# Kernel tuning notes

Hardware: AMD Instinct MI355X
Metric: run time of the kernel (lower is better)

The kernel has to match this reference:

```python
import jax, jax.numpy as jnp
import numpy as np

B, K, V = 32, 2048, 60000
D, H, L, NB = 512, 8, 4, 5
DH, M = D // H, 256  # dim_head, num random features
EPS_K = 1e-4


def _ln(x, g, b, eps=1e-5):
    mu = x.mean(-1, keepdims=True)
    var = ((x - mu) ** 2).mean(-1, keepdims=True)
    return (x - mu) / jnp.sqrt(var + eps) * g + b


def _favor_feats(x, proj, is_query):
    # FAVOR+ positive softmax-kernel features (lucidrains performer)
    dn = x.shape[-1] ** -0.25
    xd = x * dn
    dd = jnp.einsum('bhnd,md->bhnm', xd, proj)
    diag = 0.5 * jnp.sum(xd * xd, -1, keepdims=True)
    mx = jnp.max(dd, -1, keepdims=True) if is_query else jnp.max(dd)
    return (proj.shape[0] ** -0.5) * (jnp.exp(dd - diag - mx) + EPS_K)


def _orth_proj(m, d, rng):
    # gaussian orthogonal random matrix (scaling=0: chi row norms)
    blocks = []
    for _ in range(-(-m // d)):
        q, _ = np.linalg.qr(rng.standard_normal((d, d)))
        blocks.append(q.T)
    mat = np.concatenate(blocks)[:m]
    mult = np.linalg.norm(rng.standard_normal((m, d)), axis=1)
    return (mult[:, None] * mat).astype(np.float32)


def setup_inputs() -> dict:
    rng = np.random.default_rng(0)
    w = lambda *s: jnp.asarray(rng.standard_normal(s).astype(np.float32) * 0.02)
    return dict(
        expr=jnp.asarray(rng.random((B, K)).astype(np.float32)),
        coords=jnp.asarray(rng.standard_normal((B, 2)).astype(np.float32)),
        gene_ids=jnp.arange(K, dtype=jnp.int32),
        gene_table=w(V, D), pos_table=w(K, D), value_table=w(NB, D),
        sp_w=w(2, D), sp_b=jnp.zeros(D), sp_ln_g=jnp.ones(D), sp_ln_b=jnp.zeros(D),
        ln1_g=jnp.ones((L, D)), ln1_b=jnp.zeros((L, D)),
        qw=w(L, D, D), qb=jnp.zeros((L, D)), kw=w(L, D, D), kb=jnp.zeros((L, D)),
        vw=w(L, D, D), vb=jnp.zeros((L, D)), ow=w(L, D, D), ob=jnp.zeros((L, D)),
        proj=jnp.asarray(np.stack([_orth_proj(M, DH, rng) for _ in range(L)])),
        ln2_g=jnp.ones((L, D)), ln2_b=jnp.zeros((L, D)),
        ff1_w=w(L, D, 4 * D), ff1_b=jnp.zeros((L, 4 * D)),
        ff2_w=w(L, 4 * D, D), ff2_b=jnp.zeros((L, D)),
        cq_w=w(D, D), cq_b=jnp.zeros(D), ck_w=w(D, D), ck_b=jnp.zeros(D),
        cv_w=w(D, D), cv_b=jnp.zeros(D), co_w=w(D, D), co_b=jnp.zeros(D),
    )


def reference(expr, coords, gene_ids, gene_table, pos_table, value_table,
              sp_w, sp_b, sp_ln_g, sp_ln_b, ln1_g, ln1_b, qw, qb, kw, kb,
              vw, vb, ow, ob, proj, ln2_g, ln2_b, ff1_w, ff1_b, ff2_w, ff2_b,
              cq_w, cq_b, ck_w, ck_b, cv_w, cv_b, co_w, co_b):
    b, k = expr.shape
    bins = jnp.clip((expr * NB).astype(jnp.int32), 0, NB - 1)
    gene_embeds = gene_table[gene_ids][None] + pos_table[None, :k] + value_table[bins]
    sp = jax.nn.gelu(_ln(coords @ sp_w + sp_b, sp_ln_g, sp_ln_b), approximate=False)
    x = jnp.concatenate([sp[:, None, :], gene_embeds], axis=1)  # (B, K+1, D)
    n = k + 1
    for l in range(L):
        h = _ln(x, ln1_g[l], ln1_b[l])
        q = (h @ qw[l] + qb[l]).reshape(b, n, H, DH).transpose(0, 2, 1, 3)
        kk = (h @ kw[l] + kb[l]).reshape(b, n, H, DH).transpose(0, 2, 1, 3)
        v = (h @ vw[l] + vb[l]).reshape(b, n, H, DH).transpose(0, 2, 1, 3)
        qp = _favor_feats(q, proj[l], True)   # (b,h,n,M)
        kp = _favor_feats(kk, proj[l], False)
        dinv = 1.0 / jnp.einsum('bhnm,bhm->bhn', qp, kp.sum(axis=2))
        ctx = jnp.einsum('bhnm,bhnd->bhmd', kp, v)
        o = jnp.einsum('bhnm,bhmd->bhnd', qp, ctx) * dinv[..., None]
        o = o.transpose(0, 2, 1, 3).reshape(b, n, D)
        x = x + (o @ ow[l] + ob[l])
        h = _ln(x, ln2_g[l], ln2_b[l])
        x = x + jax.nn.gelu(h @ ff1_w[l] + ff1_b[l], approximate=False) @ ff2_w[l] + ff2_b[l]
    qc = x[:, :1] @ cq_w + cq_b
    kc = x[:, 1:] @ ck_w + ck_b
    vc = x[:, 1:] @ cv_w + cv_b
    attn = jax.nn.softmax(jnp.einsum('bqd,bkd->bqk', qc, kc) / (D ** 0.5), axis=-1)
    pooled = jnp.einsum('bqk,bkd->bqd', attn, vc)[:, 0]
    return pooled @ co_w + co_b
```

## Files before the change

### kernel.cpp

```cpp
#include <hip/hip_runtime.h>
#include <hip/hip_bf16.h>

#define BB 32
#define KK 2048
#define NTOK 2049
#define DD 512
#define NH 8
#define DHD 64
#define NL 4
#define MM 256
#define RTOT (BB*NTOK)
#define HROWS (RTOT/2)
#define DN 0.35355339059327373f
#define RM 0.0625f
#define EPSK 1e-4f

typedef __attribute__((ext_vector_type(8))) short bf16x8;
typedef __attribute__((ext_vector_type(4))) float f32x4;

__device__ __forceinline__ float wsum(float v) {
#pragma unroll
  for (int o = 32; o; o >>= 1) v += __shfl_xor(v, o);
  return v;
}
__device__ __forceinline__ float wmax(float v) {
#pragma unroll
  for (int o = 32; o; o >>= 1) v = fmaxf(v, __shfl_xor(v, o));
  return v;
}
__device__ __forceinline__ float gelu1(float v) {
  return 0.5f * v * (1.0f + erff(v * 0.70710678118654752f));
}
__device__ __forceinline__ float b2f(unsigned short u) {
  union { unsigned int i; float f; } w; w.i = ((unsigned int)u) << 16; return w.f;
}
__device__ __forceinline__ unsigned short f2b(float f) {
  union { float f; unsigned int i; } w; w.f = f;
  unsigned int r = w.i + 0x7FFFu + ((w.i >> 16) & 1u);
  return (unsigned short)(r >> 16);
}
__device__ __forceinline__ float4 ld4(const float* p) { return *(const float4*)p; }
__device__ __forceinline__ float4 ld4(const unsigned short* p) {
  ushort4 u = *(const ushort4*)p;
  return make_float4(b2f(u.x), b2f(u.y), b2f(u.z), b2f(u.w));
}
__device__ __forceinline__ void st4(float* p, float4 v) { *(float4*)p = v; }
__device__ __forceinline__ void st4(unsigned short* p, float4 v) {
  ushort4 u; u.x = f2b(v.x); u.y = f2b(v.y); u.z = f2b(v.z); u.w = f2b(v.w);
  *(ushort4*)p = u;
}
__device__ __forceinline__ bf16x8 ld8s(const unsigned short* p) {
  union { ushort4 u[2]; bf16x8 v; } w;
  w.u[0] = *(const ushort4*)p;
  w.u[1] = *(const ushort4*)(p + 4);
  return w.v;
}
__device__ __forceinline__ void gload16(const void* g, void* l) {
  __builtin_amdgcn_global_load_lds(
      (const __attribute__((address_space(1))) void*)g,
      (__attribute__((address_space(3))) void*)l, 16, 0, 0);
}

__global__ void sentinel_k(float* out, int n) {
  int i = blockIdx.x * 256 + threadIdx.x;
  if (i < n) out[i] = 12345.0f;
}

__global__ void biaspack_k(const float* __restrict__ a, const float* __restrict__ bsrc,
                           float* __restrict__ dst) {
  int i = threadIdx.x;
  dst[i] = a[i]; dst[i + 256] = a[i + 256];
  dst[512 + i] = bsrc[i]; dst[768 + i] = bsrc[i + 256];
}

__global__ __launch_bounds__(256) void wcvt_k(const float* __restrict__ W,
    unsigned short* __restrict__ Wt, int Kd, int Cols) {
  __shared__ float Ls[64][65];
  int tid = threadIdx.x;
  int n0 = blockIdx.x * 64, k0 = blockIdx.y * 64;
  int kr = tid >> 2, nseg = (tid & 3) << 4;
#pragma unroll
  for (int u = 0; u < 4; ++u) {
    float4 v = *(const float4*)(W + (size_t)(k0 + kr) * Cols + n0 + nseg + u * 4);
    *(float4*)&Ls[kr][nseg + u * 4] = v;
  }
  __syncthreads();
  int nr = tid >> 2, kseg = (tid & 3) << 4;
  unsigned int pk[8];
#pragma unroll
  for (int i = 0; i < 8; ++i) {
    unsigned short lo = f2b(Ls[kseg + 2 * i][nr]);
    unsigned short hi = f2b(Ls[kseg + 2 * i + 1][nr]);
    pk[i] = (unsigned int)lo | ((unsigned int)hi << 16);
  }
  unsigned short* dst = Wt + (size_t)(n0 + nr) * Kd + k0 + kseg;
  ((uint4*)dst)[0] = make_uint4(pk[0], pk[1], pk[2], pk[3]);
  ((uint4*)dst)[1] = make_uint4(pk[4], pk[5], pk[6], pk[7]);
}

__global__ __launch_bounds__(256) void embed_k(const float* __restrict__ expr,
    const int* __restrict__ gene_ids, const float* __restrict__ gene_table,
    const float* __restrict__ pos_table, const float* __restrict__ value_tab,
    float* __restrict__ x) {
  int tok = blockIdx.x * 2 + (threadIdx.x >> 7);
  int t = threadIdx.x & 127;
  int b = tok >> 11;
  int k = tok & 2047;
  float e = expr[tok];
  int bin = (int)(e * 5.0f);
  bin = bin < 0 ? 0 : (bin > 4 ? 4 : bin);
  int g = gene_ids[k];
  float4 a = ((const float4*)(gene_table + (size_t)g * DD))[t];
  float4 p = ((const float4*)(pos_table + (size_t)k * DD))[t];
  float4 vv = ((const float4*)(value_tab + (size_t)bin * DD))[t];
  float4 r;
  r.x = a.x + p.x + vv.x; r.y = a.y + p.y + vv.y;
  r.z = a.z + p.z + vv.z; r.w = a.w + p.w + vv.w;
  ((float4*)(x + ((size_t)b * NTOK + 1 + k) * DD))[t] = r;
}

__global__ __launch_bounds__(256) void sp_k(const float* __restrict__ coords,
    const float* __restrict__ sp_w, const float* __restrict__ sp_b,
    const float* __restrict__ g, const float* __restrict__ bb,
    float* __restrict__ x) {
  int b = blockIdx.x, t = threadIdx.x;
  __shared__ float red[8];
  float c0 = coords[2 * b], c1 = coords[2 * b + 1];
  float v0 = fmaf(c0, sp_w[t],       fmaf(c1, sp_w[512 + t], sp_b[t]));
  float v1 = fmaf(c0, sp_w[t + 256], fmaf(c1, sp_w[768 + t], sp_b[t + 256]));
  float s = wsum(v0 + v1);
  int wid = t >> 6;
  if ((t & 63) == 0) red[wid] = s;
  __syncthreads();
  float mu = (red[0] + red[1] + red[2] + red[3]) * (1.0f / 512.0f);
  float d0 = v0 - mu, d1 = v1 - mu;
  float s2 = wsum(d0 * d0 + d1 * d1);
  if ((t & 63) == 0) red[4 + wid] = s2;
  __syncthreads();
  float var = (red[4] + red[5] + red[6] + red[7]) * (1.0f / 512.0f);
  float rs = rsqrtf(var + 1e-5f);
  float y0 = d0 * rs * g[t] + bb[t];
  float y1 = d1 * rs * g[t + 256] + bb[t + 256];
  x[(size_t)b * NTOK * DD + t] = gelu1(y0);
  x[(size_t)b * NTOK * DD + t + 256] = gelu1(y1);
}

__global__ __launch_bounds__(128) void ln_k(const float* __restrict__ x,
    const float* __restrict__ gamma, const float* __restrict__ beta,
    unsigned short* __restrict__ h) {
  size_t row = blockIdx.x;
  int t = threadIdx.x;
  float4 v = ((const float4*)(x + row * DD))[t];
  float s = v.x + v.y + v.z + v.w;
  float s2 = v.x * v.x + v.y * v.y + v.z * v.z + v.w * v.w;
  __shared__ float red[4];
  float ws1 = wsum(s), ws2 = wsum(s2);
  int wid = t >> 6;
  if ((t & 63) == 0) { red[wid * 2] = ws1; red[wid * 2 + 1] = ws2; }
  __syncthreads();
  float S = red[0] + red[2], S2 = red[1] + red[3];
  float mu = S * (1.0f / 512.0f);
  float var = S2 * (1.0f / 512.0f) - mu * mu;
  float rs = rsqrtf(var + 1e-5f);
  float4 gm = ((const float4*)gamma)[t], bt = ((const float4*)beta)[t];
  float4 o;
  o.x = (v.x - mu) * rs * gm.x + bt.x;
  o.y = (v.y - mu) * rs * gm.y + bt.y;
  o.z = (v.z - mu) * rs * gm.z + bt.z;
  o.w = (v.w - mu) * rs * gm.w + bt.w;
  st4(h + row * DD + t * 4, o);
}

__global__ __launch_bounds__(256) void cvt_k(const float* __restrict__ x,
    unsigned short* __restrict__ o, size_t n8) {
  size_t i = (size_t)blockIdx.x * 256 + threadIdx.x;
  if (i >= n8) return;
  float4 a = ((const float4*)x)[2 * i];
  float4 b = ((const float4*)x)[2 * i + 1];
  st4(o + i * 8, a);
  st4(o + i * 8 + 4, b);
}

template <typename TC, int FLAGS>
__global__ __launch_bounds__(256) void gemm_bb(const unsigned short* __restrict__ A, long lda,
    const unsigned short* __restrict__ Wt, const float* __restrict__ bias,
    TC* __restrict__ C, int ldc, int R, int Kd) {
  __shared__ unsigned short Sh[128 * 136];
  unsigned short* As = Sh;
  unsigned short* Bs = Sh + 128 * 64;
  const int tid = threadIdx.x;
  const int lane = tid & 63;
  const int w = tid >> 6;
  const int wr = w >> 1, wc = w & 1;
  const int nwg = gridDim.x * gridDim.y;
  const int orig = blockIdx.y * gridDim.x + blockIdx.x;
  const int qd = nwg >> 3, rm = nwg & 7;
  const int xcd = orig & 7, idx = orig >> 3;
  const int wg = (xcd < rm ? xcd * (qd + 1) : rm * (qd + 1) + (xcd - rm) * qd) + idx;
  const int rblk = (wg / gridDim.x) << 7;
  const int cblk = (wg % gridDim.x) << 7;
  const int m0 = lane & 15, kb = lane >> 4;
  const int lrow8 = lane >> 3;
  const int csw = (((lane & 7) ^ lrow8) << 3);
  f32x4 acc[4][4] = {};
  for (int k0 = 0; k0 < Kd; k0 += 64) {
#pragma unroll
    for (int rd = 0; rd < 4; ++rd) {
      int rg = w * 32 + rd * 8;
      int gra = rblk + rg + lrow8; if (gra >= R) gra = R - 1;
      gload16(A  + (size_t)gra * lda + k0 + csw, &As[rg * 64]);
      gload16(Wt + (size_t)(cblk + rg + lrow8) * Kd + k0 + csw, &Bs[rg * 64]);
    }
    __syncthreads();
    bf16x8 af[2][4], bfr[2][4];
#pragma unroll
    for (int ks = 0; ks < 2; ++ks) {
      int c = (ks << 2) | kb;
#pragma unroll
      for (int mi = 0; mi < 4; ++mi) {
        int ar = wr * 64 + mi * 16 + m0;
        af[ks][mi] = *(const bf16x8*)&As[ar * 64 + ((c ^ (ar & 7)) << 3)];
        int br = wc * 64 + mi * 16 + m0;
        bfr[ks][mi] = *(const bf16x8*)&Bs[br * 64 + ((c ^ (br & 7)) << 3)];
      }
    }
#pragma unroll
    for (int ks = 0; ks < 2; ++ks)
#pragma unroll
      for (int mi = 0; mi < 4; ++mi)
#pragma unroll
        for (int ni = 0; ni < 4; ++ni)
          acc[mi][ni] = __builtin_amdgcn_mfma_f32_16x16x32_bf16(af[ks][mi], bfr[ks][ni], acc[mi][ni], 0, 0, 0);
    __syncthreads();
  }
  const int lrow4 = (lane >> 4) << 2, lcol = lane & 15;
  if constexpr (sizeof(TC) == 2) {
#pragma unroll
    for (int mi = 0; mi < 4; ++mi)
#pragma unroll
      for (int reg = 0; reg < 4; ++reg) {
        int rloc = wr * 64 + mi * 16 + lrow4 + reg;
#pragma unroll
        for (int ni = 0; ni < 4; ++ni) {
          int cloc = wc * 64 + ni * 16 + lcol;
          float v = acc[mi][ni][reg] + bias[cblk + cloc];
          if constexpr ((FLAGS & 1) != 0) v = gelu1(v);
          Sh[rloc * 136 + cloc] = f2b(v);
        }
      }
    __syncthreads();
    int rl = tid >> 1;
    int row = rblk + rl;
    if (row < R) {
      unsigned short* cp = (unsigned short*)C + (size_t)row * ldc + cblk;
#pragma unroll
      for (int u = 0; u < 8; ++u) {
        int c = (tid & 1) * 8 + u * 16;
        *(uint4*)(cp + c) = *(const uint4*)&Sh[rl * 136 + c];
      }
    }
  } else {
    float* Sf = (float*)Sh;
#pragma unroll
    for (int p = 0; p < 2; ++p) {
      if (wr == p) {
#pragma unroll
        for (int mi = 0; mi < 4; ++mi)
#pragma unroll
          for (int reg = 0; reg < 4; ++reg) {
            int rloc = mi * 16 + lrow4 + reg;
#pragma unroll
            for (int ni = 0; ni < 4; ++ni) {
              int cloc = wc * 64 + ni * 16 + lcol;
              float v = acc[mi][ni][reg] + bias[cblk + cloc];
              if constexpr ((FLAGS & 1) != 0) v = gelu1(v);
              Sf[rloc * 132 + cloc] = v;
            }
          }
      }
      __syncthreads();
      int rl = tid >> 2;
      int row = rblk + p * 64 + rl;
      if (row < R) {
        float* cp = (float*)C + (size_t)row * ldc + cblk;
#pragma unroll
        for (int u = 0; u < 8; ++u) {
          int c = (tid & 3) * 4 + u * 16;
          float4 nv = *(const float4*)&Sf[rl * 132 + c];
          if constexpr ((FLAGS & 2) != 0) {
            float4 old = *(const float4*)(cp + c);
            nv.x += old.x; nv.y += old.y; nv.z += old.z; nv.w += old.w;
          }
          *(float4*)(cp + c) = nv;
        }
      }
      __syncthreads();
    }
  }
}

template <typename TA, typename TC>
__global__ __launch_bounds__(256) void gemm_t(const TA* __restrict__ A, long lda,
    const float* __restrict__ W, const float* __restrict__ bias,
    TC* __restrict__ C, int ldc, int R, int Kd, int Cols) {
  __shared__ float As[16][68];
  __shared__ float Ws[16][64];
  int tid = threadIdx.x;
  int tx = tid & 15, ty = tid >> 4;
  int rblk = blockIdx.y << 6, cblk = blockIdx.x << 6;
  float acc[4][4] = {};
  int lr = tid >> 2, lk = (tid & 3) << 2;
  int wk = tid >> 4, wcc = (tid & 15) << 2;
  int gra = rblk + lr;
  for (int k0 = 0; k0 < Kd; k0 += 16) {
    float4 av = make_float4(0.f, 0.f, 0.f, 0.f);
    if (gra < R) av = ld4(A + (size_t)gra * lda + k0 + lk);
    As[lk][lr] = av.x; As[lk + 1][lr] = av.y; As[lk + 2][lr] = av.z; As[lk + 3][lr] = av.w;
    *(float4*)&Ws[wk][wcc] = *(const float4*)(W + (size_t)(k0 + wk) * Cols + cblk + wcc);
    __syncthreads();
#pragma unroll
    for (int p = 0; p < 16; ++p) {
      float4 a4 = *(const float4*)&As[p][ty << 2];
      float4 b4 = *(const float4*)&Ws[p][tx << 2];
      acc[0][0] = fmaf(a4.x, b4.x, acc[0][0]); acc[0][1] = fmaf(a4.x, b4.y, acc[0][1]);
      acc[0][2] = fmaf(a4.x, b4.z, acc[0][2]); acc[0][3] = fmaf(a4.x, b4.w, acc[0][3]);
      acc[1][0] = fmaf(a4.y, b4.x, acc[1][0]); acc[1][1] = fmaf(a4.y, b4.y, acc[1][1]);
      acc[1][2] = fmaf(a4.y, b4.z, acc[1][2]); acc[1][3] = fmaf(a4.y, b4.w, acc[1][3]);
      acc[2][0] = fmaf(a4.z, b4.x, acc[2][0]); acc[2][1] = fmaf(a4.z, b4.y, acc[2][1]);
      acc[2][2] = fmaf(a4.z, b4.z, acc[2][2]); acc[2][3] = fmaf(a4.z, b4.w, acc[2][3]);
      acc[3][0] = fmaf(a4.w, b4.x, acc[3][0]); acc[3][1] = fmaf(a4.w, b4.y, acc[3][1]);
      acc[3][2] = fmaf(a4.w, b4.z, acc[3][2]); acc[3][3] = fmaf(a4.w, b4.w, acc[3][3]);
    }
    __syncthreads();
  }
  int gcb = cblk + (tx << 2);
  float4 bi = *(const float4*)(bias + gcb);
#pragma unroll
  for (int i = 0; i < 4; ++i) {
    int gr = rblk + (ty << 2) + i;
    if (gr < R) {
      float4 val;
      val.x = acc[i][0] + bi.x; val.y = acc[i][1] + bi.y;
      val.z = acc[i][2] + bi.z; val.w = acc[i][3] + bi.w;
      TC* cp = C + (size_t)gr * ldc + gcb;
      st4(cp, val);
    }
  }
}

__global__ __launch_bounds__(256) void kmax_k(const unsigned short* __restrict__ kv,
    const unsigned short* __restrict__ projb, float* __restrict__ bmax) {
  int orig = blockIdx.y * gridDim.x + blockIdx.x;
  int wg = ((orig & 7) << 7) + (orig >> 3);
  int bh = wg >> 2, gy = wg & 3;
  int b = bh >> 3, hh = bh & 7;
  int tid = threadIdx.x;
  int lane = tid & 63, w = tid >> 6;
  int m0 = lane & 15, kb = lane >> 4;
  __shared__ float red[4];
  bf16x8 bp[4][2];
#pragma unroll
  for (int nf = 0; nf < 4; ++nf)
#pragma unroll
    for (int ks = 0; ks < 2; ++ks)
      bp[nf][ks] = *(const bf16x8*)(projb + (size_t)(w * 64 + nf * 16 + m0) * 64 + ks * 32 + kb * 8);
  const unsigned short* kvb = kv + (size_t)b * NTOK * 1024 + hh * 64;
  float mx = -1e30f;
  for (int t = gy; t < 65; t += 4) {
    int n0 = t * 32;
    bf16x8 aq[2][2];
#pragma unroll
    for (int mi = 0; mi < 2; ++mi) {
      int n = n0 + mi * 16 + m0; if (n >= NTOK) n = NTOK - 1;
#pragma unroll
      for (int ks = 0; ks < 2; ++ks)
        aq[mi][ks] = *(const bf16x8*)(kvb + (size_t)n * 1024 + ks * 32 + kb * 8);
    }
    f32x4 da[2][4] = {};
#pragma unroll
    for (int ks = 0; ks < 2; ++ks)
#pragma unroll
      for (int mi = 0; mi < 2; ++mi)
#pragma unroll
        for (int nf = 0; nf < 4; ++nf)
          da[mi][nf] = __builtin_amdgcn_mfma_f32_16x16x32_bf16(aq[mi][ks], bp[nf][ks], da[mi][nf], 0, 0, 0);
#pragma unroll
    for (int mi = 0; mi < 2; ++mi)
#pragma unroll
      for (int nf = 0; nf < 4; ++nf)
#pragma unroll
        for (int r = 0; r < 4; ++r)
          mx = fmaxf(mx, da[mi][nf][r]);
  }
  mx *= DN;
  mx = wmax(mx);
  if ((tid & 63) == 0) red[tid >> 6] = mx;
  __syncthreads();
  if (tid == 0)
    bmax[(size_t)bh * 4 + gy] = fmaxf(fmaxf(red[0], red[1]), fmaxf(red[2], red[3]));
}

__global__ __launch_bounds__(256) void maxred_k(const float* __restrict__ in, int n,
                                                float* __restrict__ out) {
  float m = -1e30f;
  for (int i = threadIdx.x; i < n; i += 256) m = fmaxf(m, in[i]);
  m = wmax(m);
  __shared__ float red[4];
  if ((threadIdx.x & 63) == 0) red[threadIdx.x >> 6] = m;
  __syncthreads();
  if (threadIdx.x == 0) out[0] = fmaxf(fmaxf(red[0], red[1]), fmaxf(red[2], red[3]));
}

__global__ __launch_bounds__(256) void k2_k(const unsigned short* __restrict__ kv,
    const unsigned short* __restrict__ projb,
    const float* __restrict__ kmaxg, unsigned short* __restrict__ ctxTb,
    float* __restrict__ kpsum) {
  int orig = blockIdx.y * gridDim.x + blockIdx.x;
  int wg = ((orig & 7) << 7) + (orig >> 3);
  int bh = wg >> 2, mg = wg & 3;
  int b = bh >> 3, hh = bh & 7;
  int tid = threadIdx.x;
  int lane = tid & 63, w = tid >> 6;
  int m0 = lane & 15, kb = lane >> 4;
  __shared__ __align__(16) unsigned short kpT[64 * 44];
  __shared__ __align__(16) unsigned short VT[64 * 44];
  float kmax = kmaxg[0];
  bf16x8 bp[2];
#pragma unroll
  for (int ks = 0; ks < 2; ++ks)
    bp[ks] = *(const bf16x8*)(projb + (size_t)(mg * 64 + w * 16 + m0) * 64 + ks * 32 + kb * 8);
  f32x4 acc[4] = {};
  float ksum = 0.f;
  int dv = tid & 63, tq = tid >> 6;
  const unsigned short* kvb = kv + (size_t)b * NTOK * 1024 + hh * 64;
  for (int t = 0; t < 65; ++t) {
    int n0 = t * 32;
    int tlim = NTOK - n0; if (tlim > 32) tlim = 32;
    __syncthreads();
    {
      unsigned int pk[4];
#pragma unroll
      for (int j = 0; j < 8; ++j) {
        int n = n0 + tq * 8 + j; if (n >= NTOK) n = NTOK - 1;
        unsigned int v = kvb[(size_t)n * 1024 + 512 + dv];
        if (j & 1) pk[j >> 1] |= v << 16; else pk[j >> 1] = v;
      }
      *(uint2*)&VT[dv * 44 + tq * 8]     = make_uint2(pk[0], pk[1]);
      *(uint2*)&VT[dv * 44 + tq * 8 + 4] = make_uint2(pk[2], pk[3]);
    }
    bf16x8 aq[2][2];
    float dg[2];
#pragma unroll
    for (int mi = 0; mi < 2; ++mi) {
      int n = n0 + mi * 16 + m0; if (n >= NTOK) n = NTOK - 1;
      float s = 0.f;
#pragma unroll
      for (int ks = 0; ks < 2; ++ks) {
        aq[mi][ks] = *(const bf16x8*)(kvb + (size_t)n * 1024 + ks * 32 + kb * 8);
        const unsigned short* ap = (const unsigned short*)&aq[mi][ks];
#pragma unroll
        for (int j = 0; j < 8; ++j) { float v = b2f(ap[j]); s = fmaf(v, v, s); }
      }
      s += __shfl_xor(s, 16);
      s += __shfl_xor(s, 32);
      dg[mi] = 0.5f * DN * DN * s;
    }
    f32x4 da[2] = {};
#pragma unroll
    for (int ks = 0; ks < 2; ++ks)
#pragma unroll
      for (int mi = 0; mi < 2; ++mi)
        da[mi] = __builtin_amdgcn_mfma_f32_16x16x32_bf16(aq[mi][ks], bp[ks], da[mi], 0, 0, 0);
#pragma unroll
    for (int mi = 0; mi < 2; ++mi) {
      unsigned int pk[2];
#pragma unroll
      for (int r = 0; r < 4; ++r) {
        float dval = __shfl(dg[mi], (kb << 2) | r);
        int tt = mi * 16 + (kb << 2) + r;
        float kp = 0.f;
        if (tt < tlim)
          kp = RM * (__expf(da[mi][r] * DN - dval - kmax) + EPSK);
        ksum += kp;
        unsigned int h = (unsigned int)f2b(kp);
        if (r & 1) pk[r >> 1] |= h << 16; else pk[r >> 1] = h;
      }
      *(uint2*)&kpT[(w * 16 + m0) * 44 + mi * 16 + (kb << 2)] = make_uint2(pk[0], pk[1]);
    }
    __syncthreads();
    bf16x8 af = ld8s(&kpT[(w * 16 + m0) * 44 + kb * 8]);
#pragma unroll
    for (int di = 0; di < 4; ++di) {
      bf16x8 bfv = ld8s(&VT[(di * 16 + m0) * 44 + kb * 8]);
      acc[di] = __builtin_amdgcn_mfma_f32_16x16x32_bf16(af, bfv, acc[di], 0, 0, 0);
    }
  }
  ksum += __shfl_xor(ksum, 16);
  ksum += __shfl_xor(ksum, 32);
  if (kb == 0) kpsum[(size_t)bh * MM + mg * 64 + w * 16 + m0] = ksum;
  unsigned short* cT = ctxTb + (size_t)bh * (64 * 256);
#pragma unroll
  for (int di = 0; di < 4; ++di)
#pragma unroll
    for (int r = 0; r < 4; ++r) {
      int m = mg * 64 + w * 16 + (kb << 2) + r;
      int d = di * 16 + m0;
      cT[d * 256 + m] = f2b(acc[di][r]);
    }
}

__global__ __launch_bounds__(256) void qfeat_k(unsigned short* __restrict__ kv,
    const unsigned short* __restrict__ projb,
    const unsigned short* __restrict__ ctxTb,
    const float* __restrict__ kpsum) {
  int orig = blockIdx.y * gridDim.x + blockIdx.x;
  int wg = ((orig & 7) * 416) + (orig >> 3);
  int bh = wg / 13, gy = wg % 13;
  int b = bh >> 3, hh = bh & 7;
  int tid = threadIdx.x;
  int lane = tid & 63, w = tid >> 6;
  int m0 = lane & 15, kb = lane >> 4;
  __shared__ float ddl[32 * 266];
  __shared__ unsigned short Pb[32 * 264];
  __shared__ float ksum_s[256];
  __shared__ float diag_s[32];
  __shared__ float dinv_s[32];
  ksum_s[tid] = kpsum[(size_t)bh * MM + tid];
  bf16x8 bp[4][2], bc[8];
#pragma unroll
  for (int nf = 0; nf < 4; ++nf)
#pragma unroll
    for (int ks = 0; ks < 2; ++ks)
      bp[nf][ks] = *(const bf16x8*)(projb + (size_t)(w * 64 + nf * 16 + m0) * 64 + ks * 32 + kb * 8);
  const unsigned short* cT = ctxTb + (size_t)bh * (64 * 256);
#pragma unroll
  for (int ks = 0; ks < 8; ++ks)
    bc[ks] = *(const bf16x8*)(cT + (size_t)(w * 16 + m0) * 256 + ks * 32 + kb * 8);
  unsigned short* kvb = kv + (size_t)b * NTOK * 1024 + hh * 64;
  int t8 = tid >> 3, q8 = tid & 7;
  for (int t = gy; t < 65; t += 13) {
    int n0 = t * 32;
    int tlim = NTOK - n0; if (tlim > 32) tlim = 32;
    bf16x8 aq[2][2];
#pragma unroll
    for (int mi = 0; mi < 2; ++mi) {
      int n = n0 + mi * 16 + m0; if (n >= NTOK) n = NTOK - 1;
#pragma unroll
      for (int ks = 0; ks < 2; ++ks)
        aq[mi][ks] = *(const bf16x8*)(kvb + (size_t)n * 1024 + ks * 32 + kb * 8);
    }
#pragma unroll
    for (int mi = 0; mi < 2; ++mi) {
      float s = 0.f;
      const unsigned short* ap = (const unsigned short*)&aq[mi][0];
#pragma unroll
      for (int j = 0; j < 16; ++j) { float v = b2f(ap[j]); s = fmaf(v, v, s); }
      s += __shfl_xor(s, 16); s += __shfl_xor(s, 32);
      if (w == 0 && kb == 0) diag_s[mi * 16 + m0] = 0.5f * DN * DN * s;
    }
    f32x4 da[2][4] = {};
#pragma unroll
    for (int ks = 0; ks < 2; ++ks)
#pragma unroll
      for (int mi = 0; mi < 2; ++mi)
#pragma unroll
        for (int nf = 0; nf < 4; ++nf)
          da[mi][nf] = __builtin_amdgcn_mfma_f32_16x16x32_bf16(aq[mi][ks], bp[nf][ks], da[mi][nf], 0, 0, 0);
#pragma unroll
    for (int mi = 0; mi < 2; ++mi)
#pragma unroll
      for (int nf = 0; nf < 4; ++nf)
#pragma unroll
        for (int r = 0; r < 4; ++r)
          ddl[(mi * 16 + kb * 4 + r) * 266 + w * 64 + nf * 16 + m0] = da[mi][nf][r] * DN;
    __syncthreads();
    float mx = -1e30f;
    if (t8 < tlim) {
      for (int j = 0; j < 32; ++j) mx = fmaxf(mx, ddl[t8 * 266 + q8 + 8 * j]);
    }
    mx = fmaxf(mx, __shfl_xor(mx, 1));
    mx = fmaxf(mx, __shfl_xor(mx, 2));
    mx = fmaxf(mx, __shfl_xor(mx, 4));
    float den = 0.f;
    if (t8 < tlim) {
      float dg = diag_s[t8];
      for (int j = 0; j < 32; ++j) {
        int mm = q8 + 8 * j;
        float e = RM * (__expf(ddl[t8 * 266 + mm] - dg - mx) + EPSK);
        Pb[t8 * 264 + mm] = f2b(e);
        den = fmaf(e, ksum_s[mm], den);
      }
    }
    den += __shfl_xor(den, 1); den += __shfl_xor(den, 2); den += __shfl_xor(den, 4);
    if (q8 == 0 && t8 < tlim) dinv_s[t8] = 1.0f / den;
    __syncthreads();
    f32x4 oa[2] = {};
#pragma unroll
    for (int ks = 0; ks < 8; ++ks)
#pragma unroll
      for (int mi = 0; mi < 2; ++mi) {
        bf16x8 ap = *(const bf16x8*)&Pb[(mi * 16 + m0) * 264 + ks * 32 + kb * 8];
        oa[mi] = __builtin_amdgcn_mfma_f32_16x16x32_bf16(ap, bc[ks], oa[mi], 0, 0, 0);
      }
#pragma unroll
    for (int mi = 0; mi < 2; ++mi)
#pragma unroll
      for (int r = 0; r < 4; ++r) {
        int row = mi * 16 + kb * 4 + r;
        if (row < tlim) {
          kvb[(size_t)(n0 + row) * 1024 + 512 + w * 16 + m0] =
              f2b(oa[mi][r] * dinv_s[row]);
        }
      }
    __syncthreads();
  }
}

__global__ __launch_bounds__(256) void attn_sc_k(const unsigned short* __restrict__ qc,
    const unsigned short* __restrict__ kcvc, float* __restrict__ scbuf,
    float* __restrict__ pmax) {
  int b = blockIdx.x, g = blockIdx.y, tid = threadIdx.x;
  int w = tid >> 6, lane = tid & 63;
  __shared__ float qs[DD];
  __shared__ float red[4];
  {
    ushort2 qu = ((const ushort2*)(qc + (size_t)b * DD))[tid];
    ((float2*)qs)[tid] = make_float2(b2f(qu.x), b2f(qu.y));
  }
  __syncthreads();
  float mx = -1e30f;
  for (int it = 0; it < 64; ++it) {
    int kk = g * 256 + w * 64 + it;
    const unsigned short* row = kcvc + ((size_t)b * NTOK + 1 + kk) * 1024 + lane * 8;
    float4 r0 = ld4(row), r1 = ld4(row + 4);
    float4 q0 = ((const float4*)qs)[lane * 2], q1 = ((const float4*)qs)[lane * 2 + 1];
    float s = r0.x * q0.x + r0.y * q0.y + r0.z * q0.z + r0.w * q0.w
            + r1.x * q1.x + r1.y * q1.y + r1.z * q1.z + r1.w * q1.w;
    s = wsum(s) * 0.044194173824159216f;
    if (lane == 0) scbuf[(size_t)b * KK + kk] = s;
    mx = fmaxf(mx, s);
  }
  if (lane == 0) red[w] = mx;
  __syncthreads();
  if (tid == 0) pmax[b * 8 + g] = fmaxf(fmaxf(red[0], red[1]), fmaxf(red[2], red[3]));
}
__global__ __launch_bounds__(256) void attn_w_k(const float* __restrict__ pmax,
    float* __restrict__ scbuf, float* __restrict__ pinv) {
  int b = blockIdx.x, tid = threadIdx.x;
  __shared__ float red[4];
  float mx = -1e30f;
#pragma unroll
  for (int i = 0; i < 8; ++i) mx = fmaxf(mx, pmax[b * 8 + i]);
  float sum = 0.f;
  for (int i = tid; i < KK; i += 256) {
    float e = __expf(scbuf[(size_t)b * KK + i] - mx);
    scbuf[(size_t)b * KK + i] = e;
    sum += e;
  }
  sum = wsum(sum);
  if ((tid & 63) == 0) red[tid >> 6] = sum;
  __syncthreads();
  if (tid == 0) pinv[b] = 1.0f / (red[0] + red[1] + red[2] + red[3]);
}
__global__ __launch_bounds__(256) void attn_vs_k(const float* __restrict__ scbuf,
    const unsigned short* __restrict__ kcvc, float* __restrict__ ppart) {
  int b = blockIdx.x, g = blockIdx.y, tid = threadIdx.x;
  float2 acc = {0.f, 0.f};
  for (int it = 0; it < 256; ++it) {
    int kk = g * 256 + it;
    float wgt = scbuf[(size_t)b * KK + kk];
    ushort2 vu = ((const ushort2*)(kcvc + ((size_t)b * NTOK + 1 + kk) * 1024 + 512))[tid];
    acc.x = fmaf(wgt, b2f(vu.x), acc.x);
    acc.y = fmaf(wgt, b2f(vu.y), acc.y);
  }
  ((float2*)(ppart + ((size_t)b * 8 + g) * DD))[tid] = acc;
}
__global__ __launch_bounds__(256) void attn_red_k(const float* __restrict__ ppart,
    const float* __restrict__ pinv, float* __restrict__ pooled) {
  int b = blockIdx.x, tid = threadIdx.x;
  float inv = pinv[b];
  float2 acc = {0.f, 0.f};
#pragma unroll
  for (int g = 0; g < 8; ++g) {
    float2 p = ((const float2*)(ppart + ((size_t)b * 8 + g) * DD))[tid];
    acc.x += p.x; acc.y += p.y;
  }
  ((float2*)(pooled + (size_t)b * DD))[tid] = make_float2(acc.x * inv, acc.y * inv);
}

__global__ __launch_bounds__(256) void out_k(const float* __restrict__ pooled,
    const float* __restrict__ co_w, const float* __restrict__ co_b,
    float* __restrict__ out) {
  int b = blockIdx.x, tid = threadIdx.x;
  __shared__ float ps[DD];
  ((float2*)ps)[tid] = ((const float2*)(pooled + (size_t)b * DD))[tid];
  __syncthreads();
  float a0 = co_b[tid], a1 = co_b[tid + 256];
  for (int d = 0; d < 512; ++d) {
    float p = ps[d];
    a0 = fmaf(p, co_w[(size_t)d * 512 + tid], a0);
    a1 = fmaf(p, co_w[(size_t)d * 512 + tid + 256], a1);
  }
  out[(size_t)b * 512 + tid] = a0;
  out[(size_t)b * 512 + tid + 256] = a1;
}

extern "C" void kernel_launch(void* const* d_in, const int* in_sizes, int n_in,
                              void* d_out, int out_size, void* d_ws, size_t ws_size,
                              hipStream_t stream) {
  const float* expr       = (const float*)d_in[0];
  const float* coords     = (const float*)d_in[1];
  const int*   gene_ids   = (const int*)d_in[2];
  const float* gene_table = (const float*)d_in[3];
  const float* pos_table  = (const float*)d_in[4];
  const float* value_tab  = (const float*)d_in[5];
  const float* sp_w  = (const float*)d_in[6];
  const float* sp_b  = (const float*)d_in[7];
  const float* sp_g  = (const float*)d_in[8];
  const float* sp_bb = (const float*)d_in[9];
  const float* ln1_g = (const float*)d_in[10];
  const float* ln1_b = (const float*)d_in[11];
  const float* qw = (const float*)d_in[12];
  const float* qbias = (const float*)d_in[13];
  const float* kw = (const float*)d_in[14];
  const float* kbias = (const float*)d_in[15];
  const float* vw = (const float*)d_in[16];
  const float* vbias = (const float*)d_in[17];
  const float* ow = (const float*)d_in[18];
  const float* obias = (const float*)d_in[19];
  const float* proj  = (const float*)d_in[20];
  const float* ln2_g = (const float*)d_in[21];
  const float* ln2_b = (const float*)d_in[22];
  const float* ff1w = (const float*)d_in[23];
  const float* ff1b = (const float*)d_in[24];
  const float* ff2w = (const float*)d_in[25];
  const float* ff2b = (const float*)d_in[26];
  const float* cqw = (const float*)d_in[27];
  const float* cqb = (const float*)d_in[28];
  const float* ckw = (const float*)d_in[29];
  const float* ckb = (const float*)d_in[30];
  const float* cvw = (const float*)d_in[31];
  const float* cvb = (const float*)d_in[32];
  const float* cow = (const float*)d_in[33];
  const float* cob = (const float*)d_in[34];
  float* out = (float*)d_out;

  const size_t SZ = (size_t)RTOT * DD;
  const size_t MS = (size_t)DD * DD;
  const size_t FS = (size_t)DD * 4 * DD;
  const size_t LST = 4 * MS + 2 * FS;
  const size_t WBN = 4 * LST + 2 * MS;
  const size_t CTXN = (size_t)BB * NH * 64 * 256;

  float* x = (float*)d_ws;
  unsigned short* KVb = (unsigned short*)(x + SZ);
  unsigned short* Cb = KVb + 2 * SZ;
  unsigned short* wb = Cb + SZ;
  unsigned short* ctxTb = wb + WBN;
  unsigned short* projb = ctxTb + CTXN;
  float* kpsum = (float*)(projb + (size_t)NL * MM * DHD);
  float* pooled = kpsum + (size_t)BB * NH * MM;
  float* bmax  = pooled + (size_t)BB * DD;
  float* kmaxg = bmax + 2816;
  float* scbuf = kmaxg + 16;
  float* pmax  = scbuf + (size_t)BB * KK;
  float* pinv  = pmax + 256;
  float* ppart = pinv + 32;
  float* biasKV = ppart + (size_t)BB * 8 * DD;
  unsigned short* qcb = (unsigned short*)(biasKV + (size_t)(NL + 1) * 1024);
  size_t need = (size_t)((char*)(qcb + (size_t)BB * DD) - (char*)d_ws) + 256;
  if (ws_size < need) {
    sentinel_k<<<(out_size + 255) / 256, 256, 0, stream>>>(out, out_size);
    return;
  }

  for (int l = 0; l < NL; ++l) {
    unsigned short* wl = wb + l * LST;
    wcvt_k<<<dim3(8, 8), 256, 0, stream>>>(kw + l * MS, wl,          512, 512);
    wcvt_k<<<dim3(8, 8), 256, 0, stream>>>(vw + l * MS, wl + MS,     512, 512);
    wcvt_k<<<dim3(8, 8), 256, 0, stream>>>(qw + l * MS, wl + 2 * MS, 512, 512);
    wcvt_k<<<dim3(8, 8), 256, 0, stream>>>(ow + l * MS, wl + 3 * MS, 512, 512);
    wcvt_k<<<dim3(32, 8), 256, 0, stream>>>(ff1w + l * FS, wl + 4 * MS,      512, 2048);
    wcvt_k<<<dim3(8, 32), 256, 0, stream>>>(ff2w + l * FS, wl + 4 * MS + FS, 2048, 512);
    biaspack_k<<<1, 256, 0, stream>>>(kbias + l * DD, vbias + l * DD, biasKV + l * 1024);
  }
  wcvt_k<<<dim3(8, 8), 256, 0, stream>>>(ckw, wb + 4 * LST,      512, 512);
  wcvt_k<<<dim3(8, 8), 256, 0, stream>>>(cvw, wb + 4 * LST + MS, 512, 512);
  biaspack_k<<<1, 256, 0, stream>>>(ckb, cvb, biasKV + NL * 1024);
  cvt_k<<<32, 256, 0, stream>>>(proj, projb, (size_t)NL * MM * DHD / 8);

  embed_k<<<BB * KK / 2, 256, 0, stream>>>(expr, gene_ids, gene_table, pos_table, value_tab, x);
  sp_k<<<BB, 256, 0, stream>>>(coords, sp_w, sp_b, sp_g, sp_bb, x);

  const int RB = (RTOT + 127) / 128;
  const int HB = (HROWS + 127) / 128;
  for (int l = 0; l < NL; ++l) {
    unsigned short* wl = wb + l * LST;
    const unsigned short* pbl = projb + (size_t)l * MM * DHD;
    ln_k<<<RTOT, 128, 0, stream>>>(x, ln1_g + l * DD, ln1_b + l * DD, Cb);
    gemm_bb<unsigned short, 0><<<dim3(8, RB), 256, 0, stream>>>(Cb, DD,
        wl, biasKV + l * 1024, KVb, 1024, RTOT, DD);
    kmax_k<<<dim3(256, 4), 256, 0, stream>>>(KVb, pbl, bmax);
    maxred_k<<<1, 256, 0, stream>>>(bmax, BB * NH * 4, kmaxg);
    k2_k<<<dim3(256, 4), 256, 0, stream>>>(KVb, pbl, kmaxg, ctxTb, kpsum);
    gemm_bb<unsigned short, 0><<<dim3(4, RB), 256, 0, stream>>>(Cb, DD,
        wl + 2 * MS, qbias + l * DD, KVb, 1024, RTOT, DD);
    qfeat_k<<<dim3(256, 13), 256, 0, stream>>>(KVb, pbl, ctxTb, kpsum);
    gemm_bb<float, 2><<<dim3(4, RB), 256, 0, stream>>>(KVb + 512, 1024,
        wl + 3 * MS, obias + l * DD, x, DD, RTOT, DD);
    ln_k<<<RTOT, 128, 0, stream>>>(x, ln2_g + l * DD, ln2_b + l * DD, Cb);
    for (int c = 0; c < 2; ++c) {
      gemm_bb<unsigned short, 1><<<dim3(16, HB), 256, 0, stream>>>(Cb + (size_t)c * HROWS * DD, DD,
          wl + 4 * MS, ff1b + (size_t)l * 4 * DD, KVb, 2048, HROWS, DD);
      gemm_bb<float, 2><<<dim3(4, HB), 256, 0, stream>>>(KVb, 2048,
          wl + 4 * MS + FS, ff2b + l * DD, x + (size_t)c * HROWS * DD, DD, HROWS, 2048);
    }
  }
  cvt_k<<<(int)(SZ / 8 / 256), 256, 0, stream>>>(x, Cb, SZ / 8);
  gemm_bb<unsigned short, 0><<<dim3(8, RB), 256, 0, stream>>>(Cb, DD,
      wb + 4 * LST, biasKV + NL * 1024, KVb, 1024, RTOT, DD);
  gemm_t<float, unsigned short><<<dim3(8, 1), 256, 0, stream>>>(x, (long)NTOK * DD,
      cqw, cqb, qcb, DD, BB, DD, DD);
  attn_sc_k<<<dim3(BB, 8), 256, 0, stream>>>(qcb, KVb, scbuf, pmax);
  attn_w_k<<<BB, 256, 0, stream>>>(pmax, scbuf, pinv);
  attn_vs_k<<<dim3(BB, 8), 256, 0, stream>>>(scbuf, KVb, ppart);
  attn_red_k<<<BB, 256, 0, stream>>>(ppart, pinv, pooled);
  out_k<<<BB, 256, 0, stream>>>(pooled, cow, cob, out);
}
```

Before: 5.420 ms.

## Store residual stream in bf16 and fuse Q into the K/V projection GEMM

```diff
diff --git a/kernel.cpp b/kernel.cpp
--- a/kernel.cpp
+++ b/kernel.cpp
@@ -72,6 +72,13 @@
   dst[i] = a[i]; dst[i + 256] = a[i + 256];
   dst[512 + i] = bsrc[i]; dst[768 + i] = bsrc[i + 256];
 }
+__global__ void biaspack3_k(const float* __restrict__ a, const float* __restrict__ bsrc,
+                            const float* __restrict__ c, float* __restrict__ dst) {
+  int i = threadIdx.x;
+  dst[i] = a[i]; dst[i + 256] = a[i + 256];
+  dst[512 + i] = bsrc[i]; dst[768 + i] = bsrc[i + 256];
+  dst[1024 + i] = c[i]; dst[1280 + i] = c[i + 256];
+}
 
 __global__ __launch_bounds__(256) void wcvt_k(const float* __restrict__ W,
     unsigned short* __restrict__ Wt, int Kd, int Cols) {
@@ -101,7 +108,7 @@
 __global__ __launch_bounds__(256) void embed_k(const float* __restrict__ expr,
     const int* __restrict__ gene_ids, const float* __restrict__ gene_table,
     const float* __restrict__ pos_table, const float* __restrict__ value_tab,
-    float* __restrict__ x) {
+    unsigned short* __restrict__ x) {
   int tok = blockIdx.x * 2 + (threadIdx.x >> 7);
   int t = threadIdx.x & 127;
   int b = tok >> 11;
@@ -116,13 +123,13 @@
   float4 r;
   r.x = a.x + p.x + vv.x; r.y = a.y + p.y + vv.y;
   r.z = a.z + p.z + vv.z; r.w = a.w + p.w + vv.w;
-  ((float4*)(x + ((size_t)b * NTOK + 1 + k) * DD))[t] = r;
+  st4(x + ((size_t)b * NTOK + 1 + k) * DD + t * 4, r);
 }
 
 __global__ __launch_bounds__(256) void sp_k(const float* __restrict__ coords,
     const float* __restrict__ sp_w, const float* __restrict__ sp_b,
     const float* __restrict__ g, const float* __restrict__ bb,
-    float* __restrict__ x) {
+    unsigned short* __restrict__ x) {
   int b = blockIdx.x, t = threadIdx.x;
   __shared__ float red[8];
   float c0 = coords[2 * b], c1 = coords[2 * b + 1];
@@ -141,16 +148,16 @@
   float rs = rsqrtf(var + 1e-5f);
   float y0 = d0 * rs * g[t] + bb[t];
   float y1 = d1 * rs * g[t + 256] + bb[t + 256];
-  x[(size_t)b * NTOK * DD + t] = gelu1(y0);
-  x[(size_t)b * NTOK * DD + t + 256] = gelu1(y1);
-}
-
-__global__ __launch_bounds__(128) void ln_k(const float* __restrict__ x,
+  x[(size_t)b * NTOK * DD + t] = f2b(gelu1(y0));
+  x[(size_t)b * NTOK * DD + t + 256] = f2b(gelu1(y1));
+}
+
+__global__ __launch_bounds__(128) void ln_k(const unsigned short* __restrict__ x,
     const float* __restrict__ gamma, const float* __restrict__ beta,
     unsigned short* __restrict__ h) {
   size_t row = blockIdx.x;
   int t = threadIdx.x;
-  float4 v = ((const float4*)(x + row * DD))[t];
+  float4 v = ld4(x + row * DD + t * 4);
   float s = v.x + v.y + v.z + v.w;
   float s2 = v.x * v.x + v.y * v.y + v.z * v.z + v.w * v.w;
   __shared__ float red[4];
@@ -169,16 +176,6 @@
   o.z = (v.z - mu) * rs * gm.z + bt.z;
   o.w = (v.w - mu) * rs * gm.w + bt.w;
   st4(h + row * DD + t * 4, o);
-}
-
-__global__ __launch_bounds__(256) void cvt_k(const float* __restrict__ x,
-    unsigned short* __restrict__ o, size_t n8) {
-  size_t i = (size_t)blockIdx.x * 256 + threadIdx.x;
-  if (i >= n8) return;
-  float4 a = ((const float4*)x)[2 * i];
-  float4 b = ((const float4*)x)[2 * i + 1];
-  st4(o + i * 8, a);
-  st4(o + i * 8 + 4, b);
 }
 
 template <typename TC, int FLAGS>
@@ -234,7 +231,7 @@
     __syncthreads();
   }
   const int lrow4 = (lane >> 4) << 2, lcol = lane & 15;
-  if constexpr (sizeof(TC) == 2) {
+  if constexpr (sizeof(TC) == 2 && (FLAGS & 2) == 0) {
 #pragma unroll
     for (int mi = 0; mi < 4; ++mi)
 #pragma unroll
@@ -282,16 +279,30 @@
       int rl = tid >> 2;
       int row = rblk + p * 64 + rl;
       if (row < R) {
-        float* cp = (float*)C + (size_t)row * ldc + cblk;
-#pragma unroll
-        for (int u = 0; u < 8; ++u) {
-          int c = (tid & 3) * 4 + u * 16;
-          float4 nv = *(const float4*)&Sf[rl * 132 + c];
-          if constexpr ((FLAGS & 2) != 0) {
-            float4 old = *(const float4*)(cp + c);
-            nv.x += old.x; nv.y += old.y; nv.z += old.z; nv.w += old.w;
+        if constexpr (sizeof(TC) == 4) {
+          float* cp = (float*)C + (size_t)row * ldc + cblk;
+#pragma unroll
+          for (int u = 0; u < 8; ++u) {
+            int c = (tid & 3) * 4 + u * 16;
+            float4 nv = *(const float4*)&Sf[rl * 132 + c];
+            if constexpr ((FLAGS & 2) != 0) {
+              float4 old = *(const float4*)(cp + c);
+              nv.x += old.x; nv.y += old.y; nv.z += old.z; nv.w += old.w;
+            }
+            *(float4*)(cp + c) = nv;
           }
-          *(float4*)(cp + c) = nv;
+        } else {
+          unsigned short* cp = (unsigned short*)C + (size_t)row * ldc + cblk;
+#pragma unroll
+          for (int u = 0; u < 8; ++u) {
+            int c = (tid & 3) * 4 + u * 16;
+            float4 nv = *(const float4*)&Sf[rl * 132 + c];
+            ushort4 old = *(const ushort4*)(cp + c);
+            ushort4 nw;
+            nw.x = f2b(nv.x + b2f(old.x)); nw.y = f2b(nv.y + b2f(old.y));
+            nw.z = f2b(nv.z + b2f(old.z)); nw.w = f2b(nv.w + b2f(old.w));
+            *(ushort4*)(cp + c) = nw;
+          }
         }
       }
       __syncthreads();
@@ -364,7 +375,7 @@
 #pragma unroll
     for (int ks = 0; ks < 2; ++ks)
       bp[nf][ks] = *(const bf16x8*)(projb + (size_t)(w * 64 + nf * 16 + m0) * 64 + ks * 32 + kb * 8);
-  const unsigned short* kvb = kv + (size_t)b * NTOK * 1024 + hh * 64;
+  const unsigned short* kvb = kv + (size_t)b * NTOK * 1536 + hh * 64;
   float mx = -1e30f;
   for (int t = gy; t < 65; t += 4) {
     int n0 = t * 32;
@@ -374,7 +385,7 @@
       int n = n0 + mi * 16 + m0; if (n >= NTOK) n = NTOK - 1;
 #pragma unroll
       for (int ks = 0; ks < 2; ++ks)
-        aq[mi][ks] = *(const bf16x8*)(kvb + (size_t)n * 1024 + ks * 32 + kb * 8);
+        aq[mi][ks] = *(const bf16x8*)(kvb + (size_t)n * 1536 + ks * 32 + kb * 8);
     }
     f32x4 da[2][4] = {};
 #pragma unroll
@@ -432,7 +443,7 @@
   f32x4 acc[4] = {};
   float ksum = 0.f;
   int dv = tid & 63, tq = tid >> 6;
-  const unsigned short* kvb = kv + (size_t)b * NTOK * 1024 + hh * 64;
+  const unsigned short* kvb = kv + (size_t)b * NTOK * 1536 + hh * 64;
   for (int t = 0; t < 65; ++t) {
     int n0 = t * 32;
     int tlim = NTOK - n0; if (tlim > 32) tlim = 32;
@@ -442,7 +453,7 @@
 #pragma unroll
       for (int j = 0; j < 8; ++j) {
         int n = n0 + tq * 8 + j; if (n >= NTOK) n = NTOK - 1;
-        unsigned int v = kvb[(size_t)n * 1024 + 512 + dv];
+        unsigned int v = kvb[(size_t)n * 1536 + 512 + dv];
         if (j & 1) pk[j >> 1] |= v << 16; else pk[j >> 1] = v;
       }
       *(uint2*)&VT[dv * 44 + tq * 8]     = make_uint2(pk[0], pk[1]);
@@ -456,7 +467,7 @@
       float s = 0.f;
 #pragma unroll
       for (int ks = 0; ks < 2; ++ks) {
-        aq[mi][ks] = *(const bf16x8*)(kvb + (size_t)n * 1024 + ks * 32 + kb * 8);
+        aq[mi][ks] = *(const bf16x8*)(kvb + (size_t)n * 1536 + ks * 32 + kb * 8);
         const unsigned short* ap = (const unsigned short*)&aq[mi][ks];
 #pragma unroll
         for (int j = 0; j < 8; ++j) { float v = b2f(ap[j]); s = fmaf(v, v, s); }
@@ -536,7 +547,7 @@
 #pragma unroll
   for (int ks = 0; ks < 8; ++ks)
     bc[ks] = *(const bf16x8*)(cT + (size_t)(w * 16 + m0) * 256 + ks * 32 + kb * 8);
-  unsigned short* kvb = kv + (size_t)b * NTOK * 1024 + hh * 64;
+  unsigned short* kvb = kv + (size_t)b * NTOK * 1536 + hh * 64;
   int t8 = tid >> 3, q8 = tid & 7;
   for (int t = gy; t < 65; t += 13) {
     int n0 = t * 32;
@@ -547,7 +558,7 @@
       int n = n0 + mi * 16 + m0; if (n >= NTOK) n = NTOK - 1;
 #pragma unroll
       for (int ks = 0; ks < 2; ++ks)
-        aq[mi][ks] = *(const bf16x8*)(kvb + (size_t)n * 1024 + ks * 32 + kb * 8);
+        aq[mi][ks] = *(const bf16x8*)(kvb + (size_t)n * 1536 + 1024 + ks * 32 + kb * 8);
     }
 #pragma unroll
     for (int mi = 0; mi < 2; ++mi) {
@@ -608,7 +619,7 @@
       for (int r = 0; r < 4; ++r) {
         int row = mi * 16 + kb * 4 + r;
         if (row < tlim) {
-          kvb[(size_t)(n0 + row) * 1024 + 512 + w * 16 + m0] =
+          kvb[(size_t)(n0 + row) * 1536 + w * 16 + m0] =
               f2b(oa[mi][r] * dinv_s[row]);
         }
       }
@@ -751,10 +762,11 @@
   const size_t LST = 4 * MS + 2 * FS;
   const size_t WBN = 4 * LST + 2 * MS;
   const size_t CTXN = (size_t)BB * NH * 64 * 256;
-
-  float* x = (float*)d_ws;
-  unsigned short* KVb = (unsigned short*)(x + SZ);
-  unsigned short* Cb = KVb + 2 * SZ;
+  const size_t KVQN = (size_t)RTOT * 1536;
+
+  unsigned short* x = (unsigned short*)d_ws;
+  unsigned short* KVQb = x + SZ;
+  unsigned short* Cb = KVQb + KVQN;
   unsigned short* wb = Cb + SZ;
   unsigned short* ctxTb = wb + WBN;
   unsigned short* projb = ctxTb + CTXN;
@@ -766,8 +778,8 @@
   float* pmax  = scbuf + (size_t)BB * KK;
   float* pinv  = pmax + 256;
   float* ppart = pinv + 32;
-  float* biasKV = ppart + (size_t)BB * 8 * DD;
-  unsigned short* qcb = (unsigned short*)(biasKV + (size_t)(NL + 1) * 1024);
+  float* biasKVQ = ppart + (size_t)BB * 8 * DD;
+  unsigned short* qcb = (unsigned short*)(biasKVQ + (size_t)NL * 1536 + 1024);
   size_t need = (size_t)((char*)(qcb + (size_t)BB * DD) - (char*)d_ws) + 256;
   if (ws_size < need) {
     sentinel_k<<<(out_size + 255) / 256, 256, 0, stream>>>(out, out_size);
@@ -782,12 +794,22 @@
     wcvt_k<<<dim3(8, 8), 256, 0, stream>>>(ow + l * MS, wl + 3 * MS, 512, 512);
     wcvt_k<<<dim3(32, 8), 256, 0, stream>>>(ff1w + l * FS, wl + 4 * MS,      512, 2048);
     wcvt_k<<<dim3(8, 32), 256, 0, stream>>>(ff2w + l * FS, wl + 4 * MS + FS, 2048, 512);
-    biaspack_k<<<1, 256, 0, stream>>>(kbias + l * DD, vbias + l * DD, biasKV + l * 1024);
+    biaspack3_k<<<1, 256, 0, stream>>>(kbias + l * DD, vbias + l * DD, qbias + l * DD,
+                                       biasKVQ + l * 1536);
   }
   wcvt_k<<<dim3(8, 8), 256, 0, stream>>>(ckw, wb + 4 * LST,      512, 512);
   wcvt_k<<<dim3(8, 8), 256, 0, stream>>>(cvw, wb + 4 * LST + MS, 512, 512);
-  biaspack_k<<<1, 256, 0, stream>>>(ckb, cvb, biasKV + NL * 1024);
-  cvt_k<<<32, 256, 0, stream>>>(proj, projb, (size_t)NL * MM * DHD / 8);
+  biaspack_k<<<1, 256, 0, stream>>>(ckb, cvb, biasKVQ + NL * 1536);
+  {
+    const float* p4 = proj;
+    unsigned short* pb = projb;
+    (void)p4; (void)pb;
+  }
+  {
+    struct Cvt { };
+  }
+  extern __global__ void cvtp_k(const float*, unsigned short*, size_t);
+  cvtp_k<<<32, 256, 0, stream>>>(proj, projb, (size_t)NL * MM * DHD / 8);
 
   embed_k<<<BB * KK / 2, 256, 0, stream>>>(expr, gene_ids, gene_table, pos_table, value_tab, x);
   sp_k<<<BB, 256, 0, stream>>>(coords, sp_w, sp_b, sp_g, sp_bb, x);
@@ -798,32 +820,39 @@
     unsigned short* wl = wb + l * LST;
     const unsigned short* pbl = projb + (size_t)l * MM * DHD;
     ln_k<<<RTOT, 128, 0, stream>>>(x, ln1_g + l * DD, ln1_b + l * DD, Cb);
-    gemm_bb<unsigned short, 0><<<dim3(8, RB), 256, 0, stream>>>(Cb, DD,
-        wl, biasKV + l * 1024, KVb, 1024, RTOT, DD);
-    kmax_k<<<dim3(256, 4), 256, 0, stream>>>(KVb, pbl, bmax);
+    gemm_bb<unsigned short, 0><<<dim3(12, RB), 256, 0, stream>>>(Cb, DD,
+        wl, biasKVQ + l * 1536, KVQb, 1536, RTOT, DD);
+    kmax_k<<<dim3(256, 4), 256, 0, stream>>>(KVQb, pbl, bmax);
     maxred_k<<<1, 256, 0, stream>>>(bmax, BB * NH * 4, kmaxg);
-    k2_k<<<dim3(256, 4), 256, 0, stream>>>(KVb, pbl, kmaxg, ctxTb, kpsum);
-    gemm_bb<unsigned short, 0><<<dim3(4, RB), 256, 0, stream>>>(Cb, DD,
-        wl + 2 * MS, qbias + l * DD, KVb, 1024, RTOT, DD);
-    qfeat_k<<<dim3(256, 13), 256, 0, stream>>>(KVb, pbl, ctxTb, kpsum);
-    gemm_bb<float, 2><<<dim3(4, RB), 256, 0, stream>>>(KVb + 512, 1024,
+    k2_k<<<dim3(256, 4), 256, 0, stream>>>(KVQb, pbl, kmaxg, ctxTb, kpsum);
+    qfeat_k<<<dim3(256, 13), 256, 0, stream>>>(KVQb, pbl, ctxTb, kpsum);
+    gemm_bb<unsigned short, 2><<<dim3(4, RB), 256, 0, stream>>>(KVQb, 1536,
         wl + 3 * MS, obias + l * DD, x, DD, RTOT, DD);
     ln_k<<<RTOT, 128, 0, stream>>>(x, ln2_g + l * DD, ln2_b + l * DD, Cb);
     for (int c = 0; c < 2; ++c) {
       gemm_bb<unsigned short, 1><<<dim3(16, HB), 256, 0, stream>>>(Cb + (size_t)c * HROWS * DD, DD,
-          wl + 4 * MS, ff1b + (size_t)l * 4 * DD, KVb, 2048, HROWS, DD);
-      gemm_bb<float, 2><<<dim3(4, HB), 256, 0, stream>>>(KVb, 2048,
+          wl + 4 * MS, ff1b + (size_t)l * 4 * DD, KVQb, 2048, HROWS, DD);
+      gemm_bb<unsigned short, 2><<<dim3(4, HB), 256, 0, stream>>>(KVQb, 2048,
           wl + 4 * MS + FS, ff2b + l * DD, x + (size_t)c * HROWS * DD, DD, HROWS, 2048);
     }
   }
-  cvt_k<<<(int)(SZ / 8 / 256), 256, 0, stream>>>(x, Cb, SZ / 8);
-  gemm_bb<unsigned short, 0><<<dim3(8, RB), 256, 0, stream>>>(Cb, DD,
-      wb + 4 * LST, biasKV + NL * 1024, KVb, 1024, RTOT, DD);
-  gemm_t<float, unsigned short><<<dim3(8, 1), 256, 0, stream>>>(x, (long)NTOK * DD,
+  gemm_bb<unsigned short, 0><<<dim3(8, RB), 256, 0, stream>>>(x, DD,
+      wb + 4 * LST, biasKVQ + NL * 1536, KVQb, 1024, RTOT, DD);
+  gemm_t<unsigned short, unsigned short><<<dim3(8, 1), 256, 0, stream>>>(x, (long)NTOK * DD,
       cqw, cqb, qcb, DD, BB, DD, DD);
-  attn_sc_k<<<dim3(BB, 8), 256, 0, stream>>>(qcb, KVb, scbuf, pmax);
+  attn_sc_k<<<dim3(BB, 8), 256, 0, stream>>>(qcb, KVQb, scbuf, pmax);
   attn_w_k<<<BB, 256, 0, stream>>>(pmax, scbuf, pinv);
-  attn_vs_k<<<dim3(BB, 8), 256, 0, stream>>>(scbuf, KVb, ppart);
+  attn_vs_k<<<dim3(BB, 8), 256, 0, stream>>>(scbuf, KVQb, ppart);
   attn_red_k<<<BB, 256, 0, stream>>>(ppart, pinv, pooled);
   out_k<<<BB, 256, 0, stream>>>(pooled, cow, cob, out);
 }
+
+__global__ __launch_bounds__(256) void cvtp_k(const float* __restrict__ src,
+    unsigned short* __restrict__ dst, size_t n8) {
+  size_t i = (size_t)blockIdx.x * 256 + threadIdx.x;
+  if (i >= n8) return;
+  float4 a = ((const float4*)src)[2 * i];
+  float4 b = ((const float4*)src)[2 * i + 1];
+  st4(dst + i * 8, a);
+  st4(dst + i * 8 + 4, b);
+}
```

New measurement: 5.058 ms. 6.7% less time.
